# Optimization experiments

Hardware: AMD Instinct MI355X
Metric: run time of the kernel (lower is better)

## Reference

```python
import jax, jax.numpy as jnp
import numpy as np

N = 65536      # number of nodes being updated
EMBED = 1024   # embed_size
G = 256        # g_size (per-head dim)
MLP = 256      # mlp_size
H = 4          # n_head


def setup_inputs() -> dict:
    key = jax.random.key(0)
    ks = jax.random.split(key, 8)
    s_in = 1.0 / np.sqrt(EMBED)
    s_g = 1.0 / np.sqrt(G)
    s_m = 1.0 / np.sqrt(MLP)
    s_hg = 1.0 / np.sqrt(H * G)
    return {
        "q": jax.random.normal(ks[0], (N, EMBED), jnp.float32),
        "rep": jax.random.normal(ks[1], (N, EMBED), jnp.float32),
        "Wq": jax.random.normal(ks[2], (EMBED, H * G), jnp.float32) * s_in,
        "Wk": jax.random.normal(ks[3], (EMBED, H * G), jnp.float32) * s_in,
        "Wv": jax.random.normal(ks[4], (EMBED, H * G), jnp.float32) * s_in,
        "W1": jax.random.normal(ks[5], (H, G, MLP), jnp.float32) * s_g,
        "b1": jnp.zeros((H, MLP), jnp.float32),
        "W2": jax.random.normal(ks[6], (H, MLP, G), jnp.float32) * s_m,
        "b2": jnp.zeros((H, G), jnp.float32),
        "Ws": jax.random.normal(ks[7], (H * G, EMBED), jnp.float32) * s_hg,
    }


def reference(q, rep, Wq, Wk, Wv, W1, b1, W2, b2, Ws):
    # Per-head Q/K/V projections: [N, E] -> [N, H, G]
    n = q.shape[0]
    Qh = (q @ Wq).reshape(n, H, G)
    Kh = (rep @ Wk).reshape(n, H, G)
    Vh = (rep @ Wv).reshape(n, H, G)
    # Elementwise scaled attention gate (Q, K are per-node vectors -> 2D attn)
    gate = jax.nn.sigmoid(Qh * Kh * (1.0 / np.sqrt(G)))
    z = gate * Vh  # [N, H, G]
    # Per-head MLP (num_mlp = 1 block): G -> MLP -> G with ReLU
    h1 = jax.nn.relu(jnp.einsum('nhg,hgm->nhm', z, W1) + b1)
    z2 = jnp.einsum('nhm,hmg->nhg', h1, W2) + b2
    update_gate = z2.reshape(n, H * G)
    # update_attn_scale (no bias) + fused residual: h = Q - K + proj(gate)
    h = q - rep + update_gate @ Ws
    return h
```

## Files before the change

### kernel.cpp

```cpp
#include <hip/hip_runtime.h>
#include <hip/hip_bf16.h>


typedef __attribute__((ext_vector_type(8))) short bf16x8;
typedef __attribute__((ext_vector_type(4))) float f32x4;
typedef __attribute__((ext_vector_type(4))) short short4v;

#define AS1 __attribute__((address_space(1)))
#define AS3 __attribute__((address_space(3)))

static __device__ __forceinline__ short f2b(float x) {
  __hip_bfloat16 h = __float2bfloat16(x);
  return __builtin_bit_cast(short, h);
}
static __device__ __forceinline__ float b2f(short s) {
  unsigned u = ((unsigned)(unsigned short)s) << 16;
  return __builtin_bit_cast(float, u);
}

__global__ void cvt_bf16(const float* __restrict__ in, short* __restrict__ out, long n) {
  long i = ((long)blockIdx.x * blockDim.x + threadIdx.x) * 4;
  const long stride = (long)gridDim.x * blockDim.x * 4;
  for (; i < n; i += stride) {
    float4 v = *(const float4*)(in + i);
    short4v o = { f2b(v.x), f2b(v.y), f2b(v.z), f2b(v.w) };
    *(short4v*)(out + i) = o;
  }
}

__global__ void prep_weights(
    const float* __restrict__ Wq, const float* __restrict__ Wk, const float* __restrict__ Wv,
    const float* __restrict__ W1, const float* __restrict__ W2, const float* __restrict__ Ws,
    short* __restrict__ wqt, short* __restrict__ wkt, short* __restrict__ wvt,
    short* __restrict__ w1t, short* __restrict__ w2t, short* __restrict__ wst)
{
  const int job = blockIdx.z;
  const float* src; short* dst; int R, C;
  if (job < 3)       { src = (job==0)?Wq:((job==1)?Wk:Wv); dst = (job==0)?wqt:((job==1)?wkt:wvt); R = 1024; C = 1024; }
  else if (job == 3) { src = Ws; dst = wst; R = 1024; C = 1024; }
  else if (job < 8)  { int h = job-4; src = W1 + h*65536; dst = w1t + h*65536; R = 256; C = 256; }
  else               { int h = job-8; src = W2 + h*65536; dst = w2t + h*65536; R = 256; C = 256; }
  const int c0 = blockIdx.x * 32, r0 = blockIdx.y * 32;
  if (c0 >= C || r0 >= R) return;
  __shared__ float t[32][33];
  for (int i = threadIdx.y; i < 32; i += 8)
    t[i][threadIdx.x] = src[(long)(r0 + i) * C + c0 + threadIdx.x];
  __syncthreads();
  for (int i = threadIdx.y; i < 32; i += 8)
    dst[(long)(c0 + i) * R + r0 + threadIdx.x] = f2b(t[threadIdx.x][i]);
}

template <int KDIM, int LDA, int LDB, bool RELU, bool BIAS, bool RESID, bool SWZ>
__global__ __launch_bounds__(512, 2) void gemm_bf16(
    const short* __restrict__ A, long zsa,
    const short* __restrict__ Bt, long zsb,
    void* __restrict__ outv, long ldc, long zsc,
    const float* __restrict__ bias, long zsbias,
    const short* __restrict__ qres, const short* __restrict__ rres)
{
  __shared__ __align__(16) short lA[4 * 8192];
  __shared__ __align__(16) short lB[4 * 8192];
  const int lane = threadIdx.x & 63, wave = threadIdx.x >> 6;
  const int wm = wave >> 2, wn = wave & 3;
  int bx = blockIdx.x, by = blockIdx.y;
  if (SWZ) {
    const int nbx = gridDim.x;
    const int flat = by * nbx + bx;
    const int chunk = (int)(gridDim.x * gridDim.y) >> 3;
    const int fid = (flat & 7) * chunk + (flat >> 3);
    bx = fid % nbx; by = fid / nbx;
  }
  const long bm = (long)by * 256;
  const int  bn = bx * 256;
  const int  zi = blockIdx.z;

  const short* Ab = A + (long)zi * zsa + bm * LDA;
  const short* Bb = Bt + (long)zi * zsb + (long)bn * LDB;
  constexpr int NS = KDIM / 32;
  const int g0 = lane >> 4;
  const int arow = wm * 128 + (lane & 15);
  const int bcol = wn * 64 + (lane & 15);

  const char* aP = (const char*)lA + arow * 64 + (((g0 ^ (arow >> 1)) & 3) << 4);
  const char* bP = (const char*)lB + bcol * 64 + (((g0 ^ (bcol >> 1)) & 3) << 4);

  const int rw = lane >> 2;
  const int gg = (lane & 3) ^ ((rw >> 1) & 3);
  const short* Asrc = Ab + (wave * 16 + rw) * LDA + (gg << 3);
  const short* Bsrc = Bb + (wave * 16 + rw) * LDB + (gg << 3);
  short* lAd = lA + wave * 16 * 32;
  short* lBd = lB + wave * 16 * 32;

  auto stA = [&](int slot, int s) {
    const int sc = s < NS ? s : NS - 1;
    const short* src = Asrc + sc * 32;
    short* d = lAd + slot * 8192;
    __builtin_amdgcn_global_load_lds((const AS1 void*)src,              (AS3 void*)d,        16, 0, 0);
    __builtin_amdgcn_global_load_lds((const AS1 void*)(src + 128*LDA),  (AS3 void*)(d+4096), 16, 0, 0);
  };
  auto stB = [&](int slot, int s) {
    const int sc = s < NS ? s : NS - 1;
    const short* src = Bsrc + sc * 32;
    short* d = lBd + slot * 8192;
    __builtin_amdgcn_global_load_lds((const AS1 void*)src,              (AS3 void*)d,        16, 0, 0);
    __builtin_amdgcn_global_load_lds((const AS1 void*)(src + 128*LDB),  (AS3 void*)(d+4096), 16, 0, 0);
  };

  stA(0, 0); stB(0, 0);
  stA(1, 1); stB(1, 1);
  stA(2, 2); stB(2, 2);
  asm volatile("s_waitcnt vmcnt(8)" ::: "memory");
  __builtin_amdgcn_s_barrier();

  f32x4 acc[8][4] = {};
  bf16x8 b[4];

#define PHASE(SLOT, MH, LOADB, STAGE_STMT, DOVM)                            \
  {                                                                         \
    if (LOADB) {                                                            \
      _Pragma("unroll")                                                     \
      for (int j = 0; j < 4; ++j)                                           \
        b[j] = *(const bf16x8*)(bP + (SLOT) * 16384 + j * 1024);            \
    }                                                                       \
    bf16x8 a[4];                                                            \
    _Pragma("unroll")                                                       \
    for (int i2 = 0; i2 < 4; ++i2)                                          \
      a[i2] = *(const bf16x8*)(aP + (SLOT) * 16384 + (MH) * 4096 + i2 * 1024); \
    STAGE_STMT;                                                             \
    if (DOVM) asm volatile("s_waitcnt vmcnt(8)" ::: "memory");              \
    asm volatile("" ::: "memory");                                          \
    __builtin_amdgcn_s_barrier();                                           \
    __builtin_amdgcn_s_setprio(1);                                          \
    _Pragma("unroll")                                                       \
    for (int i2 = 0; i2 < 4; ++i2)                                          \
      _Pragma("unroll")                                                     \
      for (int j = 0; j < 4; ++j)                                           \
        acc[(MH) * 4 + i2][j] = __builtin_amdgcn_mfma_f32_16x16x32_bf16(    \
            a[i2], b[j], acc[(MH) * 4 + i2][j], 0, 0, 0);                   \
    __builtin_amdgcn_s_setprio(0);                                          \
    asm volatile("" ::: "memory");                                          \
    __builtin_amdgcn_s_barrier();                                           \
  }

  for (int s = 0; s < NS; s += 4) {
    PHASE(0, 0, true,  stA(3, s + 3), false) PHASE(0, 1, false, stB(3, s + 3), true)
    PHASE(1, 0, true,  stA(0, s + 4), false) PHASE(1, 1, false, stB(0, s + 4), true)
    PHASE(2, 0, true,  stA(1, s + 5), false) PHASE(2, 1, false, stB(1, s + 5), true)
    PHASE(3, 0, true,  stA(2, s + 6), false) PHASE(3, 1, false, stB(2, s + 6), true)
  }
#undef PHASE

  #pragma unroll
  for (int i = 0; i < 8; ++i)
    #pragma unroll
    for (int j = 0; j < 4; ++j)
      #pragma unroll
      for (int r = 0; r < 4; ++r) {
        const int rl = wm * 128 + i * 16 + ((lane >> 4) << 2) + r;
        const int cl = wn * 64 + j * 16 + (lane & 15);
        float v = acc[i][j][r];
        if (BIAS) v += bias[(long)zi * zsbias + bn + cl];
        if (RELU) v = v > 0.0f ? v : 0.0f;
        const long row = bm + rl;
        const long gi = (long)zi * zsc + row * ldc + bn + cl;
        if (RESID) {
          ((float*)outv)[gi] = b2f(qres[gi]) - b2f(rres[gi]) + v;
        } else {
          ((short*)outv)[gi] = f2b(v);
        }
      }
}

__global__ __launch_bounds__(512, 2) void gemm_g23(
    const short* __restrict__ rb,
    const short* __restrict__ wkt,
    const short* __restrict__ wvt,
    const short* __restrict__ gh,
    short* __restrict__ zb)
{
  __shared__ __align__(16) short lA[4 * 8192];
  __shared__ __align__(16) short lK[4 * 4096];
  __shared__ __align__(16) short lV[4 * 4096];
  const int lane = threadIdx.x & 63, wave = threadIdx.x >> 6;
  const int wm = wave >> 2, wn = wave & 3;
  int bx = blockIdx.x, by = blockIdx.y;
  {
    const int flat = by * 8 + bx;
    const int chunk = (int)(gridDim.x * gridDim.y) >> 3;
    const int fid = (flat & 7) * chunk + (flat >> 3);
    bx = fid & 7; by = fid >> 3;
  }
  const long bm = (long)by * 256;
  const int  bn = bx * 128;

  const short* Ab = rb + bm * 1024;
  const short* Kb = wkt + (long)bn * 1024;
  const short* Vb = wvt + (long)bn * 1024;
  constexpr int NS = 32;
  const int g0 = lane >> 4;
  const int arow = wm * 128 + (lane & 15);
  const int bcol = wn * 32 + (lane & 15);

  const char* aP = (const char*)lA + arow * 64 + (((g0 ^ (arow >> 1)) & 3) << 4);
  const char* kP = (const char*)lK + bcol * 64 + (((g0 ^ (bcol >> 1)) & 3) << 4);
  const char* vP = (const char*)lV + bcol * 64 + (((g0 ^ (bcol >> 1)) & 3) << 4);

  const int rw = lane >> 2;
  const int gg = (lane & 3) ^ ((rw >> 1) & 3);
  const short* Asrc = Ab + (wave * 16 + rw) * 1024 + (gg << 3);
  const short* Ksrc = Kb + (wave * 16 + rw) * 1024 + (gg << 3);
  const short* Vsrc = Vb + (wave * 16 + rw) * 1024 + (gg << 3);
  short* lAd = lA + wave * 16 * 32;
  short* lKd = lK + wave * 16 * 32;
  short* lVd = lV + wave * 16 * 32;

  auto stA = [&](int slot, int s) {
    const int sc = s < NS ? s : NS - 1;
    const short* src = Asrc + sc * 32;
    short* d = lAd + slot * 8192;
    __builtin_amdgcn_global_load_lds((const AS1 void*)src,               (AS3 void*)d,        16, 0, 0);
    __builtin_amdgcn_global_load_lds((const AS1 void*)(src + 128*1024),  (AS3 void*)(d+4096), 16, 0, 0);
  };
  auto stKV = [&](int slot, int s) {
    const int sc = s < NS ? s : NS - 1;
    __builtin_amdgcn_global_load_lds((const AS1 void*)(Ksrc + sc * 32), (AS3 void*)(lKd + slot * 4096), 16, 0, 0);
    __builtin_amdgcn_global_load_lds((const AS1 void*)(Vsrc + sc * 32), (AS3 void*)(lVd + slot * 4096), 16, 0, 0);
  };

  stA(0, 0); stKV(0, 0);
  stA(1, 1); stKV(1, 1);
  stA(2, 2); stKV(2, 2);
  asm volatile("s_waitcnt vmcnt(8)" ::: "memory");
  __builtin_amdgcn_s_barrier();

  f32x4 ack[8][2] = {};
  f32x4 acv[8][2] = {};
  bf16x8 bk[2], bv[2];

#define PHASEG(SLOT, MH, LOADB, STAGE_STMT, DOVM)                           \
  {                                                                         \
    if (LOADB) {                                                            \
      _Pragma("unroll")                                                     \
      for (int j = 0; j < 2; ++j) {                                         \
        bk[j] = *(const bf16x8*)(kP + (SLOT) * 8192 + j * 1024);            \
        bv[j] = *(const bf16x8*)(vP + (SLOT) * 8192 + j * 1024);            \
      }                                                                     \
    }                                                                       \
    bf16x8 a[4];                                                            \
    _Pragma("unroll")                                                       \
    for (int i2 = 0; i2 < 4; ++i2)                                          \
      a[i2] = *(const bf16x8*)(aP + (SLOT) * 16384 + (MH) * 4096 + i2 * 1024); \
    STAGE_STMT;                                                             \
    if (DOVM) asm volatile("s_waitcnt vmcnt(8)" ::: "memory");              \
    asm volatile("" ::: "memory");                                          \
    __builtin_amdgcn_s_barrier();                                           \
    __builtin_amdgcn_s_setprio(1);                                          \
    _Pragma("unroll")                                                       \
    for (int i2 = 0; i2 < 4; ++i2)                                          \
      _Pragma("unroll")                                                     \
      for (int j = 0; j < 2; ++j) {                                         \
        ack[(MH) * 4 + i2][j] = __builtin_amdgcn_mfma_f32_16x16x32_bf16(    \
            a[i2], bk[j], ack[(MH) * 4 + i2][j], 0, 0, 0);                  \
        acv[(MH) * 4 + i2][j] = __builtin_amdgcn_mfma_f32_16x16x32_bf16(    \
            a[i2], bv[j], acv[(MH) * 4 + i2][j], 0, 0, 0);                  \
      }                                                                     \
    __builtin_amdgcn_s_setprio(0);                                          \
    asm volatile("" ::: "memory");                                          \
    __builtin_amdgcn_s_barrier();                                           \
  }

  for (int s = 0; s < NS; s += 4) {
    PHASEG(0, 0, true,  stA(3, s + 3), false) PHASEG(0, 1, false, stKV(3, s + 3), true)
    PHASEG(1, 0, true,  stA(0, s + 4), false) PHASEG(1, 1, false, stKV(0, s + 4), true)
    PHASEG(2, 0, true,  stA(1, s + 5), false) PHASEG(2, 1, false, stKV(1, s + 5), true)
    PHASEG(3, 0, true,  stA(2, s + 6), false) PHASEG(3, 1, false, stKV(2, s + 6), true)
  }
#undef PHASEG

  #pragma unroll
  for (int i = 0; i < 8; ++i)
    #pragma unroll
    for (int j = 0; j < 2; ++j)
      #pragma unroll
      for (int r = 0; r < 4; ++r) {
        const int rl = wm * 128 + i * 16 + ((lane >> 4) << 2) + r;
        const int cl = wn * 32 + j * 16 + (lane & 15);
        const long gi = (bm + rl) * 1024 + bn + cl;
        const float x = b2f(gh[gi]) * ack[i][j][r] * 0.0625f;
        const float gate = 1.0f / (1.0f + __expf(-x));
        zb[gi] = f2b(gate * acv[i][j][r]);
      }
}

extern "C" void kernel_launch(void* const* d_in, const int* in_sizes, int n_in,
                              void* d_out, int out_size, void* d_ws, size_t ws_size,
                              hipStream_t stream) {
  const float* q   = (const float*)d_in[0];
  const float* rep = (const float*)d_in[1];
  const float* Wq  = (const float*)d_in[2];
  const float* Wk  = (const float*)d_in[3];
  const float* Wv  = (const float*)d_in[4];
  const float* W1  = (const float*)d_in[5];
  const float* b1  = (const float*)d_in[6];
  const float* W2  = (const float*)d_in[7];
  const float* b2  = (const float*)d_in[8];
  const float* Ws  = (const float*)d_in[9];
  float* out = (float*)d_out;

  const long NE = 67108864L;
  char* ws = (char*)d_ws;
  short* qb  = (short*)(ws);
  short* rb  = (short*)(ws + NE * 2);
  short* gh  = (short*)(ws + NE * 4);
  short* zb  = (short*)(ws + NE * 6);
  short* h1b = gh;
  short* ugb = zb;
  char*  wp  = ws + NE * 8;
  short* wqt = (short*)(wp);
  short* wkt = (short*)(wp + 2097152);
  short* wvt = (short*)(wp + 4194304);
  short* wst = (short*)(wp + 6291456);
  short* w1t = (short*)(wp + 8388608);
  short* w2t = (short*)(wp + 8912896);

  cvt_bf16<<<4096, 256, 0, stream>>>(q,   qb, NE);
  cvt_bf16<<<4096, 256, 0, stream>>>(rep, rb, NE);
  prep_weights<<<dim3(32, 32, 12), dim3(32, 8), 0, stream>>>(
      Wq, Wk, Wv, W1, W2, Ws, wqt, wkt, wvt, w1t, w2t, wst);

  gemm_bf16<1024, 1024, 1024, false, false, false, true><<<dim3(4, 256), 512, 0, stream>>>(
      qb, 0, wqt, 0, gh, 1024, 0, nullptr, 0, nullptr, nullptr);
  gemm_g23<<<dim3(8, 256), 512, 0, stream>>>(rb, wkt, wvt, gh, zb);

  gemm_bf16<256, 1024, 256, true, true, false, false><<<dim3(1, 256, 4), 512, 0, stream>>>(
      zb, 256, w1t, 65536, h1b, 1024, 256, b1, 256, nullptr, nullptr);
  gemm_bf16<256, 1024, 256, false, true, false, false><<<dim3(1, 256, 4), 512, 0, stream>>>(
      h1b, 256, w2t, 65536, ugb, 1024, 256, b2, 256, nullptr, nullptr);
  gemm_bf16<1024, 1024, 1024, false, false, true, true><<<dim3(4, 256), 512, 0, stream>>>(
      ugb, 0, wst, 0, out, 1024, 0, nullptr, 0, qb, rb);
}
```

Baseline: 1.046 ms.

## Fuse per-head MLP GEMMs into one kernel keeping hidden activations in LDS

Replaces the two per-head MLP GEMM launches with one kernel. It computes z@W1+b1 with ReLU, stashes the bf16 hidden tile in swizzled LDS, then multiplies by W2 from a double-buffered LDS tile. This removes the HBM write and read of the hidden activation and one launch. It also merges the two fp32-to-bf16 conversion launches into one. The large LDS footprint limits occupancy to one block per CU.

```diff
diff --git a/kernel.cpp b/kernel.cpp
--- a/kernel.cpp
+++ b/kernel.cpp
@@ -18,7 +18,10 @@
   return __builtin_bit_cast(float, u);
 }
 
-__global__ void cvt_bf16(const float* __restrict__ in, short* __restrict__ out, long n) {
+__global__ void cvt_bf16_2(const float* __restrict__ q, const float* __restrict__ rep,
+                           short* __restrict__ qb, short* __restrict__ rb, long n) {
+  const float* __restrict__ in = blockIdx.z ? rep : q;
+  short* __restrict__ out = blockIdx.z ? rb : qb;
   long i = ((long)blockIdx.x * blockDim.x + threadIdx.x) * 4;
   const long stride = (long)gridDim.x * blockDim.x * 4;
   for (; i < n; i += stride) {
@@ -172,10 +175,8 @@
 }
 
 __global__ __launch_bounds__(512, 2) void gemm_g23(
-    const short* __restrict__ rb,
-    const short* __restrict__ wkt,
-    const short* __restrict__ wvt,
-    const short* __restrict__ gh,
+    const short* __restrict__ rb, const short* __restrict__ wkt,
+    const short* __restrict__ wvt, const short* __restrict__ gh,
     short* __restrict__ zb)
 {
   __shared__ __align__(16) short lA[4 * 8192];
@@ -292,6 +293,186 @@
       }
 }
 
+__global__ __launch_bounds__(512) void gemm_mlp(
+    const short* __restrict__ zb, const short* __restrict__ w1t,
+    const short* __restrict__ w2t, const float* __restrict__ b1,
+    const float* __restrict__ b2, short* __restrict__ ug)
+{
+  __shared__ __align__(16) char smem[163840];
+  short* lA = (short*)smem;
+  short* lB = (short*)(smem + 65536);
+  short* stash = (short*)smem;
+  short* w2b = (short*)(smem + 131072);
+
+  const int lane = threadIdx.x & 63, wave = threadIdx.x >> 6;
+  const int wm = wave >> 2, wn = wave & 3;
+  const long bm = (long)blockIdx.y * 256;
+  const int head = blockIdx.z;
+
+  const int g0 = lane >> 4;
+  const int arow = wm * 128 + (lane & 15);
+  const int bcol = wn * 64 + (lane & 15);
+  const int rw = lane >> 2;
+  const int gg = (lane & 3) ^ ((rw >> 1) & 3);
+
+  {
+    const short* Ab = zb + bm * 1024 + head * 256;
+    const short* Bb = w1t + head * 65536;
+    const char* aP = (const char*)lA + arow * 64 + (((g0 ^ (arow >> 1)) & 3) << 4);
+    const char* bP = (const char*)lB + bcol * 64 + (((g0 ^ (bcol >> 1)) & 3) << 4);
+    const short* Asrc = Ab + (wave * 16 + rw) * 1024 + (gg << 3);
+    const short* Bsrc = Bb + (wave * 16 + rw) * 256 + (gg << 3);
+    short* lAd = lA + wave * 16 * 32;
+    short* lBd = lB + wave * 16 * 32;
+
+    auto stA = [&](int slot, int s) {
+      const int sc = s < 8 ? s : 7;
+      const short* src = Asrc + sc * 32;
+      short* d = lAd + slot * 8192;
+      __builtin_amdgcn_global_load_lds((const AS1 void*)src,              (AS3 void*)d,        16, 0, 0);
+      __builtin_amdgcn_global_load_lds((const AS1 void*)(src + 128*1024), (AS3 void*)(d+4096), 16, 0, 0);
+    };
+    auto stB = [&](int slot, int s) {
+      const int sc = s < 8 ? s : 7;
+      const short* src = Bsrc + sc * 32;
+      short* d = lBd + slot * 8192;
+      __builtin_amdgcn_global_load_lds((const AS1 void*)src,              (AS3 void*)d,        16, 0, 0);
+      __builtin_amdgcn_global_load_lds((const AS1 void*)(src + 128*256),  (AS3 void*)(d+4096), 16, 0, 0);
+    };
+
+    stA(0, 0); stB(0, 0);
+    stA(1, 1); stB(1, 1);
+    stA(2, 2); stB(2, 2);
+    asm volatile("s_waitcnt vmcnt(8)" ::: "memory");
+    __builtin_amdgcn_s_barrier();
+
+    f32x4 acc[8][4] = {};
+    bf16x8 b[4];
+
+#define PHASE1(SLOT, MH, LOADB, STAGE_STMT, DOVM)                           \
+    {                                                                       \
+      if (LOADB) {                                                          \
+        _Pragma("unroll")                                                   \
+        for (int j = 0; j < 4; ++j)                                         \
+          b[j] = *(const bf16x8*)(bP + (SLOT) * 16384 + j * 1024);          \
+      }                                                                     \
+      bf16x8 a[4];                                                          \
+      _Pragma("unroll")                                                     \
+      for (int i2 = 0; i2 < 4; ++i2)                                        \
+        a[i2] = *(const bf16x8*)(aP + (SLOT) * 16384 + (MH) * 4096 + i2 * 1024); \
+      STAGE_STMT;                                                           \
+      if (DOVM) asm volatile("s_waitcnt vmcnt(8)" ::: "memory");            \
+      asm volatile("" ::: "memory");                                        \
+      __builtin_amdgcn_s_barrier();                                         \
+      __builtin_amdgcn_s_setprio(1);                                        \
+      _Pragma("unroll")                                                     \
+      for (int i2 = 0; i2 < 4; ++i2)                                        \
+        _Pragma("unroll")                                                   \
+        for (int j = 0; j < 4; ++j)                                         \
+          acc[(MH) * 4 + i2][j] = __builtin_amdgcn_mfma_f32_16x16x32_bf16(  \
+              a[i2], b[j], acc[(MH) * 4 + i2][j], 0, 0, 0);                 \
+      __builtin_amdgcn_s_setprio(0);                                        \
+      asm volatile("" ::: "memory");                                        \
+      __builtin_amdgcn_s_barrier();                                         \
+    }
+
+    for (int s = 0; s < 8; s += 4) {
+      PHASE1(0, 0, true,  stA(3, s + 3), false) PHASE1(0, 1, false, stB(3, s + 3), true)
+      PHASE1(1, 0, true,  stA(0, s + 4), false) PHASE1(1, 1, false, stB(0, s + 4), true)
+      PHASE1(2, 0, true,  stA(1, s + 5), false) PHASE1(2, 1, false, stB(1, s + 5), true)
+      PHASE1(3, 0, true,  stA(2, s + 6), false) PHASE1(3, 1, false, stB(2, s + 6), true)
+    }
+#undef PHASE1
+
+    __syncthreads();
+    #pragma unroll
+    for (int i = 0; i < 8; ++i)
+      #pragma unroll
+      for (int j = 0; j < 4; ++j)
+        #pragma unroll
+        for (int r = 0; r < 4; ++r) {
+          const int rl = wm * 128 + i * 16 + ((lane >> 4) << 2) + r;
+          const int cl = wn * 64 + j * 16 + (lane & 15);
+          float v = acc[i][j][r] + b1[head * 256 + cl];
+          v = v > 0.0f ? v : 0.0f;
+          stash[rl * 256 + ((((cl >> 3) ^ rl) & 31) << 3) + (cl & 7)] = f2b(v);
+        }
+    __syncthreads();
+  }
+
+  {
+    const short* Wb = w2t + head * 65536;
+    const short* Bsrc2 = Wb + (wave * 16 + rw) * 256 + (gg << 3);
+    short* lBd2 = w2b + wave * 16 * 32;
+    const char* b2P = (const char*)w2b + bcol * 64 + (((g0 ^ (bcol >> 1)) & 3) << 4);
+
+    auto stW = [&](int slot, int s) {
+      const int sc = s < 8 ? s : 7;
+      const short* src = Bsrc2 + sc * 32;
+      short* d = lBd2 + slot * 8192;
+      __builtin_amdgcn_global_load_lds((const AS1 void*)src,             (AS3 void*)d,        16, 0, 0);
+      __builtin_amdgcn_global_load_lds((const AS1 void*)(src + 128*256), (AS3 void*)(d+4096), 16, 0, 0);
+    };
+
+    stW(0, 0);
+    asm volatile("s_waitcnt vmcnt(0)" ::: "memory");
+    __builtin_amdgcn_s_barrier();
+
+    f32x4 acc2[8][4] = {};
+    bf16x8 br[4];
+
+    for (int s = 0; s < 8; ++s) {
+      const int sl = s & 1;
+      const int ks = s * 4 + g0;
+
+#define PHASE2(MH, LOADB, STAGE_STMT, DOVM)                                 \
+      {                                                                     \
+        if (LOADB) {                                                        \
+          _Pragma("unroll")                                                 \
+          for (int j = 0; j < 4; ++j)                                       \
+            br[j] = *(const bf16x8*)(b2P + sl * 16384 + j * 1024);          \
+        }                                                                   \
+        bf16x8 a[4];                                                        \
+        _Pragma("unroll")                                                   \
+        for (int i2 = 0; i2 < 4; ++i2) {                                    \
+          const int row = arow + (MH) * 64 + i2 * 16;                       \
+          a[i2] = *(const bf16x8*)(stash + row * 256 + (((ks ^ row) & 31) << 3)); \
+        }                                                                   \
+        STAGE_STMT;                                                         \
+        if (DOVM) asm volatile("s_waitcnt vmcnt(0)" ::: "memory");          \
+        asm volatile("" ::: "memory");                                      \
+        __builtin_amdgcn_s_barrier();                                       \
+        __builtin_amdgcn_s_setprio(1);                                      \
+        _Pragma("unroll")                                                   \
+        for (int i2 = 0; i2 < 4; ++i2)                                      \
+          _Pragma("unroll")                                                 \
+          for (int j = 0; j < 4; ++j)                                       \
+            acc2[(MH) * 4 + i2][j] = __builtin_amdgcn_mfma_f32_16x16x32_bf16( \
+                a[i2], br[j], acc2[(MH) * 4 + i2][j], 0, 0, 0);             \
+        __builtin_amdgcn_s_setprio(0);                                      \
+        asm volatile("" ::: "memory");                                      \
+        __builtin_amdgcn_s_barrier();                                       \
+      }
+
+      PHASE2(0, true,  stW(sl ^ 1, s + 1), false)
+      PHASE2(1, false, {}, true)
+#undef PHASE2
+    }
+
+    #pragma unroll
+    for (int i = 0; i < 8; ++i)
+      #pragma unroll
+      for (int j = 0; j < 4; ++j)
+        #pragma unroll
+        for (int r = 0; r < 4; ++r) {
+          const int rl = wm * 128 + i * 16 + ((lane >> 4) << 2) + r;
+          const int cl = wn * 64 + j * 16 + (lane & 15);
+          const float v = acc2[i][j][r] + b2[head * 256 + cl];
+          ug[(bm + rl) * 1024 + head * 256 + cl] = f2b(v);
+        }
+  }
+}
+
 extern "C" void kernel_launch(void* const* d_in, const int* in_sizes, int n_in,
                               void* d_out, int out_size, void* d_ws, size_t ws_size,
                               hipStream_t stream) {
@@ -313,8 +494,7 @@
   short* rb  = (short*)(ws + NE * 2);
   short* gh  = (short*)(ws + NE * 4);
   short* zb  = (short*)(ws + NE * 6);
-  short* h1b = gh;
-  short* ugb = zb;
+  short* ugb = gh;
   char*  wp  = ws + NE * 8;
   short* wqt = (short*)(wp);
   short* wkt = (short*)(wp + 2097152);
@@ -323,19 +503,14 @@
   short* w1t = (short*)(wp + 8388608);
   short* w2t = (short*)(wp + 8912896);
 
-  cvt_bf16<<<4096, 256, 0, stream>>>(q,   qb, NE);
-  cvt_bf16<<<4096, 256, 0, stream>>>(rep, rb, NE);
+  cvt_bf16_2<<<dim3(2048, 1, 2), 256, 0, stream>>>(q, rep, qb, rb, NE);
   prep_weights<<<dim3(32, 32, 12), dim3(32, 8), 0, stream>>>(
       Wq, Wk, Wv, W1, W2, Ws, wqt, wkt, wvt, w1t, w2t, wst);
 
   gemm_bf16<1024, 1024, 1024, false, false, false, true><<<dim3(4, 256), 512, 0, stream>>>(
       qb, 0, wqt, 0, gh, 1024, 0, nullptr, 0, nullptr, nullptr);
   gemm_g23<<<dim3(8, 256), 512, 0, stream>>>(rb, wkt, wvt, gh, zb);
-
-  gemm_bf16<256, 1024, 256, true, true, false, false><<<dim3(1, 256, 4), 512, 0, stream>>>(
-      zb, 256, w1t, 65536, h1b, 1024, 256, b1, 256, nullptr, nullptr);
-  gemm_bf16<256, 1024, 256, false, true, false, false><<<dim3(1, 256, 4), 512, 0, stream>>>(
-      h1b, 256, w2t, 65536, ugb, 1024, 256, b2, 256, nullptr, nullptr);
+  gemm_mlp<<<dim3(1, 256, 4), 512, 0, stream>>>(zb, w1t, w2t, b1, b2, ugb);
   gemm_bf16<1024, 1024, 1024, false, false, true, true><<<dim3(4, 256), 512, 0, stream>>>(
       ugb, 0, wst, 0, out, 1024, 0, nullptr, 0, qb, rb);
 }
```

Result: faster. 1.002 ms, median of 2 (-4.2%).
